# Optimization experiments

Hardware: AMD Instinct MI355X
Metric: run time of the kernel (lower is better)

## Reference

```python
import jax, jax.numpy as jnp
import numpy as np

N_HEADS = 32
N_KV_HEADS = 8
HEAD_DIM = 128
DIM = 4096
ROPE_THETA = 500000.0
BSZ, SEQLEN = 4, 1024


def _rope(t, cos, sin):
    # t: [B,S,H,hd]; cos/sin: [S,hd//2]
    te = t[..., 0::2]
    to = t[..., 1::2]
    c = cos[None, :, None, :]
    s = sin[None, :, None, :]
    out = jnp.stack([te * c - to * s, te * s + to * c], axis=-1)
    return out.reshape(t.shape)


def setup_inputs() -> dict:
    key = jax.random.key(0)
    ks = jax.random.split(key, 8)
    scale = 1.0 / np.sqrt(DIM)
    x = jax.random.normal(ks[0], (BSZ, SEQLEN, DIM), dtype=jnp.float32)
    wq = jax.random.normal(ks[1], (DIM, N_HEADS * HEAD_DIM), dtype=jnp.float32) * scale
    wk = jax.random.normal(ks[2], (DIM, N_KV_HEADS * HEAD_DIM), dtype=jnp.float32) * scale
    wv = jax.random.normal(ks[3], (DIM, N_KV_HEADS * HEAD_DIM), dtype=jnp.float32) * scale
    wo = jax.random.normal(ks[4], (N_HEADS * HEAD_DIM, DIM), dtype=jnp.float32) * scale
    # rotary tables: freqs_cis[s, j] = exp(i * s * theta^(-2j/hd))
    inv_freq = 1.0 / (ROPE_THETA ** (np.arange(0, HEAD_DIM, 2, dtype=np.float32) / HEAD_DIM))
    ang = np.outer(np.arange(SEQLEN, dtype=np.float32), inv_freq)
    freqs_cos = jnp.asarray(np.cos(ang), dtype=jnp.float32)
    freqs_sin = jnp.asarray(np.sin(ang), dtype=jnp.float32)
    # additive causal mask: 0 on/below diag, -inf above
    causal_mask = jnp.triu(jnp.full((SEQLEN, SEQLEN), -jnp.inf, dtype=jnp.float32), k=1)
    return {"x": x, "wq": wq, "wk": wk, "wv": wv, "wo": wo,
            "freqs_cos": freqs_cos, "freqs_sin": freqs_sin,
            "causal_mask": causal_mask, "fixed_point_iter": 0, "start_pos": 0}


def reference(x, wq, wk, wv, wo, freqs_cos, freqs_sin, causal_mask, fixed_point_iter, start_pos):
    B, S, _ = x.shape
    n_rep = N_HEADS // N_KV_HEADS
    xq = (x @ wq).reshape(B, S, N_HEADS, HEAD_DIM)
    xk = (x @ wk).reshape(B, S, N_KV_HEADS, HEAD_DIM)
    xv = (x @ wv).reshape(B, S, N_KV_HEADS, HEAD_DIM)
    xq = _rope(xq, freqs_cos, freqs_sin)
    xk = _rope(xk, freqs_cos, freqs_sin)
    # start_pos == 0 prefill: cache slice [:start_pos+S] equals freshly written xk/xv
    keys = jnp.repeat(xk, n_rep, axis=2)    # [B,S,H,hd]
    values = jnp.repeat(xv, n_rep, axis=2)
    scores = jnp.einsum('bqhd,bkhd->bhqk', xq, keys) / np.sqrt(HEAD_DIM)
    scores = scores + causal_mask  # broadcast [S,S]
    probs = jax.nn.softmax(scores.astype(jnp.float32), axis=-1).astype(xq.dtype)
    out = jnp.einsum('bhqk,bkhd->bqhd', probs, values)
    out = out.reshape(B, S, N_HEADS * HEAD_DIM)
    return out @ wo
```

## Files before the change

### kernel.cpp

```cpp
#include <hip/hip_runtime.h>

#define BSZ_  4
#define SEQ_  1024
#define NH_   32
#define NKVH_ 8
#define HD_   128
#define DIM_  4096
#define NTOK_ (BSZ_ * SEQ_)
#define QKVW_ 6144

typedef float  floatx4  __attribute__((ext_vector_type(4)));
typedef float  floatx16 __attribute__((ext_vector_type(16)));
typedef __bf16 bf16x8   __attribute__((ext_vector_type(8)));
typedef unsigned short ushortx8 __attribute__((ext_vector_type(8)));

__device__ __forceinline__ float fast_exp2(float x) {
  return __builtin_amdgcn_exp2f(x);
}

__device__ __forceinline__ unsigned short f2bf_bits(float f) {
  unsigned int u = __float_as_uint(f);
  u += 0x7FFFu + ((u >> 16) & 1u);
  return (unsigned short)(u >> 16);
}
__device__ __forceinline__ unsigned int pack_bf2_rne(float lo, float hi_) {
  return (unsigned int)f2bf_bits(lo) | ((unsigned int)f2bf_bits(hi_) << 16);
}
__device__ __forceinline__ unsigned int pack_bf2_trunc(float lo, float hi_) {
  return __builtin_amdgcn_perm(__float_as_uint(hi_), __float_as_uint(lo), 0x07060302u);
}

__device__ __forceinline__ void gld16(const void* g, void* l) {
  __builtin_amdgcn_global_load_lds(
      (const __attribute__((address_space(1))) void*)g,
      (__attribute__((address_space(3))) void*)l, 16, 0, 0);
}

__global__ __launch_bounds__(256)
void xconv(const float* __restrict__ X, unsigned short* __restrict__ XB)
{
  size_t i = ((size_t)blockIdx.x * 256 + threadIdx.x) * 4;
  float4 v = *(const float4*)&X[i];
  ushort4 o;
  o.x = f2bf_bits(v.x); o.y = f2bf_bits(v.y);
  o.z = f2bf_bits(v.z); o.w = f2bf_bits(v.w);
  *(ushort4*)&XB[i] = o;
}

__global__ __launch_bounds__(256)
void wtrans(const float* __restrict__ W, unsigned short* __restrict__ WT,
            int K, int N)
{
  __shared__ unsigned short T[32][36];
  const int k0 = blockIdx.y * 32, n0 = blockIdx.x * 32;
  const int t = threadIdx.x;
  {
    int kr = t >> 3, nc = (t & 7) * 4;
    float4 v = *(const float4*)&W[(size_t)(k0 + kr) * N + n0 + nc];
    T[kr][nc + 0] = f2bf_bits(v.x);
    T[kr][nc + 1] = f2bf_bits(v.y);
    T[kr][nc + 2] = f2bf_bits(v.z);
    T[kr][nc + 3] = f2bf_bits(v.w);
  }
  __syncthreads();
  {
    int nr = t >> 3, kc = (t & 7) * 4;
    ushort4 o;
    o.x = T[kc + 0][nr]; o.y = T[kc + 1][nr];
    o.z = T[kc + 2][nr]; o.w = T[kc + 3][nr];
    *(ushort4*)&WT[(size_t)(n0 + nr) * K + k0 + kc] = o;
  }
}

__global__ __launch_bounds__(256)
void vtrans2(const unsigned short* __restrict__ qkv, unsigned short* __restrict__ VT)
{
  __shared__ unsigned short T[32][36];
  const int bh = blockIdx.z;
  const int s0 = blockIdx.x * 32, d0 = blockIdx.y * 32;
  const int b = bh >> 3, kvh = bh & 7;
  const int t = threadIdx.x;
  {
    int sr = t >> 3, dc = (t & 7) * 4;
    ushort4 v = *(const ushort4*)&qkv[(size_t)(b * SEQ_ + s0 + sr) * QKVW_ + 5120 + kvh * HD_ + d0 + dc];
    T[sr][dc + 0] = v.x; T[sr][dc + 1] = v.y;
    T[sr][dc + 2] = v.z; T[sr][dc + 3] = v.w;
  }
  __syncthreads();
  {
    int dr = t >> 3, sc = (t & 7) * 4;
    ushort4 o;
    o.x = T[sc + 0][dr]; o.y = T[sc + 1][dr];
    o.z = T[sc + 2][dr]; o.w = T[sc + 3][dr];
    *(ushort4*)&VT[((size_t)bh * HD_ + d0 + dr) * SEQ_ + s0 + sc] = o;
  }
}

__global__ __launch_bounds__(256)
void rope2(unsigned int* __restrict__ t, const float* __restrict__ cosf,
           const float* __restrict__ sinf, int shift, int stride_u32, int base_u32)
{
  int idx = blockIdx.x * 256 + threadIdx.x;
  int tok = idx >> shift;
  int rem = idx & ((1 << shift) - 1);
  int d2  = idx & 63;
  int pos = tok & (SEQ_ - 1);
  unsigned int* p = &t[(size_t)tok * stride_u32 + base_u32 + rem];
  unsigned int pv = *p;
  float xe = __uint_as_float(pv << 16);
  float xo = __uint_as_float(pv & 0xFFFF0000u);
  float cv = cosf[pos * 64 + d2];
  float sv = sinf[pos * 64 + d2];
  float oe = xe * cv - xo * sv;
  float oo = xe * sv + xo * cv;
  *p = pack_bf2_rne(oe, oo);
}

template<bool OUT_BF16>
__global__ __launch_bounds__(512, 2)
void gemm_bt8(const unsigned short* __restrict__ A,
              const unsigned short* __restrict__ B,
              void* __restrict__ Cout, int M, int N, int K)
{
  __shared__ __align__(16) unsigned short As[4][256][32];
  __shared__ __align__(16) unsigned short Bs[4][256][32];

  const int tid  = threadIdx.x;
  const int w    = tid >> 6;
  const int lane = tid & 63;
  const int l16  = lane & 15;
  const int quad = lane >> 4;
  const int wr   = w >> 2;
  const int wc   = w & 3;

  int wg = blockIdx.x;
  const int q8 = gridDim.x >> 3;
  wg = (wg & 7) * q8 + (wg >> 3);
  const int nbx = N >> 8;
  const int bm = (wg / nbx) * 256;
  const int bn = (wg % nbx) * 256;

  const int srow     = w * 16 + (lane >> 2);
  const int cs_stage = (lane & 3) ^ ((srow >> 1) & 3);
  const int ntiles   = K >> 5;

  auto stageA = [&](int kt, int buf) {
#pragma unroll
    for (int r = 0; r < 2; r++)
      gld16(&A[(size_t)(bm + r * 128 + srow) * K + (kt << 5) + cs_stage * 8],
            (char*)&As[buf][0][0] + r * 8192 + w * 1024);
  };
  auto stageB = [&](int kt, int buf) {
#pragma unroll
    for (int r = 0; r < 2; r++)
      gld16(&B[(size_t)(bn + r * 128 + srow) * K + (kt << 5) + cs_stage * 8],
            (char*)&Bs[buf][0][0] + r * 8192 + w * 1024);
  };

  floatx4 acc[8][4];
#pragma unroll
  for (int i = 0; i < 8; i++)
#pragma unroll
    for (int j = 0; j < 4; j++) acc[i][j] = (floatx4){0.f, 0.f, 0.f, 0.f};

  const int sfrag = (l16 >> 1) & 3;
  const int cfr   = quad ^ sfrag;

#pragma unroll
  for (int t = 0; t < 3; t++) { stageA(t, t); stageB(t, t); }
  asm volatile("s_waitcnt vmcnt(8)" ::: "memory");
  __builtin_amdgcn_s_barrier();

  for (int t = 0; t < ntiles; t++) {
    const int buf  = t & 3;
    const int pbuf = (t + 3) & 3;
    const int pk   = (t + 3 < ntiles) ? (t + 3) : 0;
    const unsigned short* Ab = &As[buf][0][0];
    const unsigned short* Bb = &Bs[buf][0][0];

    bf16x8 bfr[4], af0[4], af1[4];
#pragma unroll
    for (int nj = 0; nj < 4; nj++)
      bfr[nj] = *(const bf16x8*)&Bb[(wc * 64 + nj * 16 + l16) * 32 + cfr * 8];
#pragma unroll
    for (int i = 0; i < 4; i++)
      af0[i] = *(const bf16x8*)&Ab[(wr * 128 + i * 16 + l16) * 32 + cfr * 8];
    stageA(pk, pbuf);
    __builtin_amdgcn_s_barrier();
    __builtin_amdgcn_s_setprio(1);
#pragma unroll
    for (int i = 0; i < 4; i++)
#pragma unroll
      for (int nj = 0; nj < 4; nj++)
        acc[i][nj] = __builtin_amdgcn_mfma_f32_16x16x32_bf16(af0[i], bfr[nj], acc[i][nj], 0, 0, 0);
    __builtin_amdgcn_s_setprio(0);
    __builtin_amdgcn_s_barrier();

#pragma unroll
    for (int i = 0; i < 4; i++)
      af1[i] = *(const bf16x8*)&Ab[(wr * 128 + (4 + i) * 16 + l16) * 32 + cfr * 8];
    stageB(pk, pbuf);
    __builtin_amdgcn_s_barrier();
    __builtin_amdgcn_s_setprio(1);
#pragma unroll
    for (int i = 0; i < 4; i++)
#pragma unroll
      for (int nj = 0; nj < 4; nj++)
        acc[4 + i][nj] = __builtin_amdgcn_mfma_f32_16x16x32_bf16(af1[i], bfr[nj], acc[4 + i][nj], 0, 0, 0);
    __builtin_amdgcn_s_setprio(0);
    asm volatile("s_waitcnt vmcnt(8)" ::: "memory");
    __builtin_amdgcn_s_barrier();
  }

#pragma unroll
  for (int mi = 0; mi < 8; mi++)
#pragma unroll
    for (int nj = 0; nj < 4; nj++)
#pragma unroll
      for (int r = 0; r < 4; r++) {
        size_t row = bm + wr * 128 + mi * 16 + quad * 4 + r;
        size_t col = bn + wc * 64 + nj * 16 + l16;
        if (OUT_BF16)
          ((unsigned short*)Cout)[row * N + col] = f2bf_bits(acc[mi][nj][r]);
        else
          ((float*)Cout)[row * N + col] = acc[mi][nj][r];
      }
}

__global__ __launch_bounds__(256, 2)
void flash_attn2(const unsigned short* __restrict__ qkv,
                 const unsigned short* __restrict__ vt,
                 unsigned short* __restrict__ o)
{
  __shared__ __align__(16) unsigned short S_[4][8192];
  unsigned short* Ks = &S_[0][0];
  unsigned short* Vs = &S_[1][0];

  const int bid = blockIdx.x;
  const int grp = bid >> 7;
  const int idx = bid & 127;
  const int qt = (grp == 0) ? 3 : (grp == 1) ? 2 : (grp == 2) ? 0 : 1;
  const int h = idx & 31, b = idx >> 5;

  const int kvh = h >> 2;
  const int tid = threadIdx.x, w = tid >> 6, lane = tid & 63;
  const int l31 = lane & 31, hi = lane >> 5;
  const int qb = qt * 256, qw = qb + w * 64;
  unsigned short* Ps = &S_[2][0] + w * 4096;

  const float CEXP = (float)(0.08838834764831845 * 1.4426950408889634);

  bf16x8 qf[2][8];
#pragma unroll
  for (int t2 = 0; t2 < 2; t2++) {
    const unsigned short* qrow =
        &qkv[(size_t)(b * SEQ_ + qw + t2 * 32 + l31) * QKVW_ + h * HD_ + hi * 8];
#pragma unroll
    for (int s = 0; s < 8; s++)
      qf[t2][s] = *(const bf16x8*)&qrow[s * 16];
  }

  floatx16 oa[2][4];
#pragma unroll
  for (int t2 = 0; t2 < 2; t2++)
#pragma unroll
    for (int dt = 0; dt < 4; dt++)
#pragma unroll
      for (int r = 0; r < 16; r++) oa[t2][dt][r] = 0.f;

  float ms[2] = {-3.0e38f, -3.0e38f};
  float ls[2] = {0.f, 0.f};

  const int nk = qb + 256;
  const int qmaxw = qw + 63;

  ushortx8 kreg[4], vreg[4];
  const size_t kg0 = (size_t)(b * SEQ_) * QKVW_ + 4096 + kvh * HD_;
  const size_t vg0 = ((size_t)(b * NKVH_ + kvh) * HD_) * SEQ_;
  const int krow = tid >> 4, kc = tid & 15;
  const int vrow = tid >> 3, vc = tid & 7;

  auto issue_loads = [&](int kb) {
    const size_t gb = kg0 + (size_t)kb * QKVW_;
#pragma unroll
    for (int it = 0; it < 4; it++)
      kreg[it] = *(const ushortx8*)&qkv[gb + (size_t)(it * 16 + krow) * QKVW_ + kc * 8];
    const size_t vb = vg0 + kb;
#pragma unroll
    for (int it = 0; it < 4; it++)
      vreg[it] = *(const ushortx8*)&vt[vb + (size_t)(it * 32 + vrow) * SEQ_ + vc * 8];
  };
  auto write_lds = [&]() {
#pragma unroll
    for (int it = 0; it < 4; it++) {
      int key = it * 16 + krow;
      *(ushortx8*)&Ks[key * 128 + ((kc ^ (key & 15)) * 8)] = kreg[it];
    }
#pragma unroll
    for (int it = 0; it < 4; it++) {
      int d = it * 32 + vrow;
      *(ushortx8*)&Vs[d * 64 + ((vc ^ (d & 7)) * 8)] = vreg[it];
    }
  };

  issue_loads(0);

  for (int kb_ = 0; kb_ < nk; kb_ += 64) {
    __syncthreads();
    write_lds();
    if (kb_ + 64 < nk) issue_loads(kb_ + 64);
    asm volatile("s_waitcnt lgkmcnt(0)" ::: "memory");
    __builtin_amdgcn_s_barrier();

    if (kb_ <= qmaxw) {
      const bool needmask = (kb_ + 63 > qw);

#pragma unroll
      for (int t2 = 0; t2 < 2; t2++) {
        floatx16 sc[2];
#pragma unroll
        for (int r = 0; r < 16; r++) { sc[0][r] = 0.f; sc[1][r] = 0.f; }
        __builtin_amdgcn_s_setprio(1);
#pragma unroll
        for (int s = 0; s < 8; s++) {
          int c = 2 * s + hi;
          bf16x8 k0 = *(const bf16x8*)&Ks[l31 * 128 + ((c ^ (l31 & 15)) * 8)];
          bf16x8 k1 = *(const bf16x8*)&Ks[(32 + l31) * 128 + ((c ^ ((32 + l31) & 15)) * 8)];
          sc[0] = __builtin_amdgcn_mfma_f32_32x32x16_bf16(k0, qf[t2][s], sc[0], 0, 0, 0);
          sc[1] = __builtin_amdgcn_mfma_f32_32x32x16_bf16(k1, qf[t2][s], sc[1], 0, 0, 0);
        }
        __builtin_amdgcn_s_setprio(0);

        if (needmask) {
          const int q = qw + t2 * 32 + l31;
#pragma unroll
          for (int k2 = 0; k2 < 2; k2++)
#pragma unroll
            for (int r = 0; r < 16; r++) {
              int key = kb_ + k2 * 32 + (r & 3) + 8 * (r >> 2) + 4 * hi;
              if (key > q) sc[k2][r] = -3.0e38f;
            }
        }

        float mx0 = sc[0][0], mx1 = sc[0][1];
#pragma unroll
        for (int r = 2; r < 16; r += 2) { mx0 = fmaxf(mx0, sc[0][r]); mx1 = fmaxf(mx1, sc[0][r + 1]); }
#pragma unroll
        for (int r = 0; r < 16; r += 2) { mx0 = fmaxf(mx0, sc[1][r]); mx1 = fmaxf(mx1, sc[1][r + 1]); }
        float mx = fmaxf(mx0, mx1);
        mx = fmaxf(mx, __shfl_xor(mx, 32));
        float mxs = mx * CEXP;

        float mn, alpha;
        if (__all(mxs - ms[t2] <= 8.0f)) {
          mn = ms[t2]; alpha = 1.0f;
        } else {
          mn = fmaxf(ms[t2], mxs);
          alpha = fast_exp2(ms[t2] - mn);
          ms[t2] = mn;
        }

        float rs0 = 0.f, rs1 = 0.f;
        const int qloc = t2 * 32 + l31;
#pragma unroll
        for (int k2 = 0; k2 < 2; k2++) {
          unsigned int pk[8];
#pragma unroll
          for (int r = 0; r < 16; r += 2) {
            float p0 = fast_exp2(__builtin_fmaf(sc[k2][r],     CEXP, -mn));
            float p1 = fast_exp2(__builtin_fmaf(sc[k2][r + 1], CEXP, -mn));
            rs0 += p0; rs1 += p1;
            pk[r >> 1] = pack_bf2_trunc(p0, p1);
          }
#pragma unroll
          for (int rq = 0; rq < 4; rq++) {
            int keyoff = k2 * 32 + 8 * rq + 4 * hi;
            int c = keyoff >> 3;
            uint2 val = {pk[rq * 2], pk[rq * 2 + 1]};
            *(uint2*)&Ps[qloc * 64 + ((c ^ (qloc & 7)) * 8) + (keyoff & 7)] = val;
          }
        }
        float rs = rs0 + rs1;
        rs += __shfl_xor(rs, 32);
        ls[t2] = ls[t2] * alpha + rs;

        if (__any(alpha != 1.0f)) {
#pragma unroll
          for (int dt = 0; dt < 4; dt++)
#pragma unroll
            for (int r = 0; r < 16; r++) oa[t2][dt][r] *= alpha;
        }
      }

      __builtin_amdgcn_s_setprio(1);
#pragma unroll
      for (int ks = 0; ks < 4; ks++) {
        int c = 2 * ks + hi;
        bf16x8 pf0, pf1;
        {
          int q0l = l31;
          int q1l = 32 + l31;
          pf0 = *(const bf16x8*)&Ps[q0l * 64 + ((c ^ (q0l & 7)) * 8)];
          pf1 = *(const bf16x8*)&Ps[q1l * 64 + ((c ^ (q1l & 7)) * 8)];
        }
#pragma unroll
        for (int dt = 0; dt < 4; dt++) {
          int d = dt * 32 + l31;
          bf16x8 vf = *(const bf16x8*)&Vs[d * 64 + ((c ^ (d & 7)) * 8)];
          oa[0][dt] = __builtin_amdgcn_mfma_f32_32x32x16_bf16(vf, pf0, oa[0][dt], 0, 0, 0);
          oa[1][dt] = __builtin_amdgcn_mfma_f32_32x32x16_bf16(vf, pf1, oa[1][dt], 0, 0, 0);
        }
      }
      __builtin_amdgcn_s_setprio(0);
    }
  }

  __syncthreads();
  unsigned short* patch = &S_[w][0];
  float inv[2] = {1.0f / ls[0], 1.0f / ls[1]};
#pragma unroll
  for (int t2 = 0; t2 < 2; t2++) {
    const int qloc = t2 * 32 + l31;
#pragma unroll
    for (int dt = 0; dt < 4; dt++)
#pragma unroll
      for (int rq = 0; rq < 4; rq++) {
        float a0 = oa[t2][dt][rq * 4 + 0] * inv[t2];
        float a1 = oa[t2][dt][rq * 4 + 1] * inv[t2];
        float a2 = oa[t2][dt][rq * 4 + 2] * inv[t2];
        float a3 = oa[t2][dt][rq * 4 + 3] * inv[t2];
        int doff = dt * 32 + 8 * rq + 4 * hi;
        int c = doff >> 3;
        uint2 val = {pack_bf2_rne(a0, a1), pack_bf2_rne(a2, a3)};
        *(uint2*)&patch[qloc * 128 + ((c ^ (qloc & 7)) * 8) + (doff & 7)] = val;
      }
  }
#pragma unroll
  for (int it = 0; it < 16; it++) {
    int idx2 = it * 64 + lane;
    int row = idx2 >> 4, c = idx2 & 15;
    int cc = (c & 7) ^ (row & 7);
    int cs = (c & 8) | cc;
    ushortx8 vv = *(const ushortx8*)&patch[row * 128 + cs * 8];
    *(ushortx8*)&o[(size_t)(b * SEQ_ + qb + w * 64 + row) * 4096 + h * HD_ + c * 8] = vv;
  }
}

extern "C" void kernel_launch(void* const* d_in, const int* in_sizes, int n_in,
                              void* d_out, int out_size, void* d_ws, size_t ws_size,
                              hipStream_t stream)
{
  const float* x  = (const float*)d_in[0];
  const float* wq = (const float*)d_in[1];
  const float* wk = (const float*)d_in[2];
  const float* wv = (const float*)d_in[3];
  const float* wo = (const float*)d_in[4];
  const float* fc = (const float*)d_in[5];
  const float* fs = (const float*)d_in[6];
  float* out = (float*)d_out;

  unsigned short* xb    = (unsigned short*)d_ws;
  unsigned short* wqkvT = xb    + (size_t)NTOK_ * DIM_;
  unsigned short* qkvb  = wqkvT + (size_t)QKVW_ * DIM_;
  unsigned short* vtb   = qkvb  + (size_t)NTOK_ * QKVW_;
  unsigned short* ab    = xb;
  unsigned short* woT   = wqkvT;

  dim3 blk(256);

  xconv<<<(NTOK_ * DIM_ / 4) / 256, blk, 0, stream>>>(x, xb);
  wtrans<<<dim3(DIM_ / 32, DIM_ / 32), blk, 0, stream>>>(wq, wqkvT, DIM_, DIM_);
  wtrans<<<dim3((NKVH_ * HD_) / 32, DIM_ / 32), blk, 0, stream>>>(wk, wqkvT + (size_t)4096 * DIM_, DIM_, NKVH_ * HD_);
  wtrans<<<dim3((NKVH_ * HD_) / 32, DIM_ / 32), blk, 0, stream>>>(wv, wqkvT + (size_t)5120 * DIM_, DIM_, NKVH_ * HD_);

  gemm_bt8<true><<<dim3((QKVW_ / 256) * (NTOK_ / 256)), dim3(512), 0, stream>>>(
      xb, wqkvT, qkvb, NTOK_, QKVW_, DIM_);

  wtrans<<<dim3(DIM_ / 32, DIM_ / 32), blk, 0, stream>>>(wo, woT, DIM_, DIM_);

  rope2<<<(NTOK_ * 2048) / 256, blk, 0, stream>>>((unsigned int*)qkvb, fc, fs, 11, 3072, 0);
  rope2<<<(NTOK_ * 512) / 256, blk, 0, stream>>>((unsigned int*)qkvb, fc, fs, 9, 3072, 2048);

  vtrans2<<<dim3(SEQ_ / 32, HD_ / 32, BSZ_ * NKVH_), blk, 0, stream>>>(qkvb, vtb);

  flash_attn2<<<dim3((SEQ_ / 256) * NH_ * BSZ_), blk, 0, stream>>>(qkvb, vtb, ab);

  gemm_bt8<false><<<dim3((DIM_ / 256) * (NTOK_ / 256)), dim3(512), 0, stream>>>(
      ab, woT, out, NTOK_, DIM_, DIM_);
}
```

Measured before the change: 717.3 us.

## Split GEMM 256x256 tile across 16 waves instead of 8

After: 703.6 us. About the same (-1.9%).

```diff
diff --git a/kernel.cpp b/kernel.cpp
--- a/kernel.cpp
+++ b/kernel.cpp
@@ -117,8 +117,8 @@
 }
 
 template<bool OUT_BF16>
-__global__ __launch_bounds__(512, 2)
-void gemm_bt8(const unsigned short* __restrict__ A,
+__global__ __launch_bounds__(1024, 4)
+void gemm_w16(const unsigned short* __restrict__ A,
               const unsigned short* __restrict__ B,
               void* __restrict__ Cout, int M, int N, int K)
 {
@@ -140,90 +140,80 @@
   const int bm = (wg / nbx) * 256;
   const int bn = (wg % nbx) * 256;
 
-  const int srow     = w * 16 + (lane >> 2);
-  const int cs_stage = (lane & 3) ^ ((srow >> 1) & 3);
-  const int ntiles   = K >> 5;
-
-  auto stageA = [&](int kt, int buf) {
-#pragma unroll
-    for (int r = 0; r < 2; r++)
-      gld16(&A[(size_t)(bm + r * 128 + srow) * K + (kt << 5) + cs_stage * 8],
-            (char*)&As[buf][0][0] + r * 8192 + w * 1024);
+  const int srow = tid >> 2;
+  const int scs  = (tid & 3) ^ ((srow >> 1) & 3);
+  const unsigned short* Ag = &A[(size_t)(bm + srow) * K + scs * 8];
+  const unsigned short* Bg = &B[(size_t)(bn + srow) * K + scs * 8];
+  char* AsW = (char*)&As[0][0][0] + w * 1024;
+  char* BsW = (char*)&Bs[0][0][0] + w * 1024;
+
+  const int ntiles = K >> 5;
+
+  auto stage = [&](int kt, int buf) {
+    size_t ko = (size_t)kt << 5;
+    gld16(Ag + ko, AsW + buf * 16384);
+    gld16(Bg + ko, BsW + buf * 16384);
   };
-  auto stageB = [&](int kt, int buf) {
-#pragma unroll
-    for (int r = 0; r < 2; r++)
-      gld16(&B[(size_t)(bn + r * 128 + srow) * K + (kt << 5) + cs_stage * 8],
-            (char*)&Bs[buf][0][0] + r * 8192 + w * 1024);
-  };
-
-  floatx4 acc[8][4];
-#pragma unroll
-  for (int i = 0; i < 8; i++)
+
+  floatx4 acc[4][4];
+#pragma unroll
+  for (int i = 0; i < 4; i++)
 #pragma unroll
     for (int j = 0; j < 4; j++) acc[i][j] = (floatx4){0.f, 0.f, 0.f, 0.f};
 
-  const int sfrag = (l16 >> 1) & 3;
-  const int cfr   = quad ^ sfrag;
-
-#pragma unroll
-  for (int t = 0; t < 3; t++) { stageA(t, t); stageB(t, t); }
-  asm volatile("s_waitcnt vmcnt(8)" ::: "memory");
+  const int cfr = quad ^ ((l16 >> 1) & 3);
+  const unsigned short* ArF = &As[0][wr * 64][cfr * 8];
+  const unsigned short* BrF = &Bs[0][wc * 64][cfr * 8];
+
+  stage(0, 0); stage(1, 1); stage(2, 2);
+  asm volatile("s_waitcnt vmcnt(4)" ::: "memory");
   __builtin_amdgcn_s_barrier();
 
+#pragma unroll 1
   for (int t = 0; t < ntiles; t++) {
-    const int buf  = t & 3;
-    const int pbuf = (t + 3) & 3;
-    const int pk   = (t + 3 < ntiles) ? (t + 3) : 0;
-    const unsigned short* Ab = &As[buf][0][0];
-    const unsigned short* Bb = &Bs[buf][0][0];
-
-    bf16x8 bfr[4], af0[4], af1[4];
-#pragma unroll
-    for (int nj = 0; nj < 4; nj++)
-      bfr[nj] = *(const bf16x8*)&Bb[(wc * 64 + nj * 16 + l16) * 32 + cfr * 8];
+    const int buf = t & 3;
+
+    bf16x8 af[4], bfr[4];
+    {
+      const unsigned short* Ab = ArF + (size_t)buf * (256 * 32) + l16 * 32;
+      const unsigned short* Bb = BrF + (size_t)buf * (256 * 32) + l16 * 32;
+#pragma unroll
+      for (int i = 0; i < 4; i++) af[i]  = *(const bf16x8*)&Ab[i * (16 * 32)];
+#pragma unroll
+      for (int j = 0; j < 4; j++) bfr[j] = *(const bf16x8*)&Bb[j * (16 * 32)];
+    }
+
+    {
+      int pk = (t + 3 < ntiles) ? t + 3 : 0;
+      stage(pk, (t + 3) & 3);
+    }
+
+    __builtin_amdgcn_s_setprio(1);
 #pragma unroll
     for (int i = 0; i < 4; i++)
-      af0[i] = *(const bf16x8*)&Ab[(wr * 128 + i * 16 + l16) * 32 + cfr * 8];
-    stageA(pk, pbuf);
+#pragma unroll
+      for (int j = 0; j < 4; j++)
+        acc[i][j] = __builtin_amdgcn_mfma_f32_16x16x32_bf16(af[i], bfr[j], acc[i][j], 0, 0, 0);
+    __builtin_amdgcn_s_setprio(0);
+
+    asm volatile("s_waitcnt vmcnt(4)" ::: "memory");
     __builtin_amdgcn_s_barrier();
-    __builtin_amdgcn_s_setprio(1);
-#pragma unroll
-    for (int i = 0; i < 4; i++)
-#pragma unroll
-      for (int nj = 0; nj < 4; nj++)
-        acc[i][nj] = __builtin_amdgcn_mfma_f32_16x16x32_bf16(af0[i], bfr[nj], acc[i][nj], 0, 0, 0);
-    __builtin_amdgcn_s_setprio(0);
-    __builtin_amdgcn_s_barrier();
-
-#pragma unroll
-    for (int i = 0; i < 4; i++)
-      af1[i] = *(const bf16x8*)&Ab[(wr * 128 + (4 + i) * 16 + l16) * 32 + cfr * 8];
-    stageB(pk, pbuf);
-    __builtin_amdgcn_s_barrier();
-    __builtin_amdgcn_s_setprio(1);
-#pragma unroll
-    for (int i = 0; i < 4; i++)
-#pragma unroll
-      for (int nj = 0; nj < 4; nj++)
-        acc[4 + i][nj] = __builtin_amdgcn_mfma_f32_16x16x32_bf16(af1[i], bfr[nj], acc[4 + i][nj], 0, 0, 0);
-    __builtin_amdgcn_s_setprio(0);
-    asm volatile("s_waitcnt vmcnt(8)" ::: "memory");
-    __builtin_amdgcn_s_barrier();
-  }
-
-#pragma unroll
-  for (int mi = 0; mi < 8; mi++)
-#pragma unroll
-    for (int nj = 0; nj < 4; nj++)
+  }
+
+  asm volatile("s_waitcnt vmcnt(0)" ::: "memory");
+
+#pragma unroll
+  for (int i = 0; i < 4; i++)
+#pragma unroll
+    for (int j = 0; j < 4; j++)
 #pragma unroll
       for (int r = 0; r < 4; r++) {
-        size_t row = bm + wr * 128 + mi * 16 + quad * 4 + r;
-        size_t col = bn + wc * 64 + nj * 16 + l16;
+        size_t row = bm + wr * 64 + i * 16 + quad * 4 + r;
+        size_t col = bn + wc * 64 + j * 16 + l16;
         if (OUT_BF16)
-          ((unsigned short*)Cout)[row * N + col] = f2bf_bits(acc[mi][nj][r]);
+          ((unsigned short*)Cout)[row * N + col] = f2bf_bits(acc[i][j][r]);
         else
-          ((float*)Cout)[row * N + col] = acc[mi][nj][r];
+          ((float*)Cout)[row * N + col] = acc[i][j][r];
       }
 }
 
@@ -473,7 +463,7 @@
   wtrans<<<dim3((NKVH_ * HD_) / 32, DIM_ / 32), blk, 0, stream>>>(wk, wqkvT + (size_t)4096 * DIM_, DIM_, NKVH_ * HD_);
   wtrans<<<dim3((NKVH_ * HD_) / 32, DIM_ / 32), blk, 0, stream>>>(wv, wqkvT + (size_t)5120 * DIM_, DIM_, NKVH_ * HD_);
 
-  gemm_bt8<true><<<dim3((QKVW_ / 256) * (NTOK_ / 256)), dim3(512), 0, stream>>>(
+  gemm_w16<true><<<dim3((QKVW_ / 256) * (NTOK_ / 256)), dim3(1024), 0, stream>>>(
       xb, wqkvT, qkvb, NTOK_, QKVW_, DIM_);
 
   wtrans<<<dim3(DIM_ / 32, DIM_ / 32), blk, 0, stream>>>(wo, woT, DIM_, DIM_);
@@ -485,6 +475,6 @@
 
   flash_attn2<<<dim3((SEQ_ / 256) * NH_ * BSZ_), blk, 0, stream>>>(qkvb, vtb, ab);
 
-  gemm_bt8<false><<<dim3((DIM_ / 256) * (NTOK_ / 256)), dim3(512), 0, stream>>>(
+  gemm_w16<false><<<dim3((DIM_ / 256) * (NTOK_ / 256)), dim3(1024), 0, stream>>>(
       ab, woT, out, NTOK_, DIM_, DIM_);
 }
```
